# Kernel tuning notes

Measured on AMD Instinct MI355X. Metric: run time of the kernel, lower is better.

## Reference

```python
import jax, jax.numpy as jnp
import numpy as np
from functools import partial

EPS = 1e-5

def batchnorm(x, gamma, beta):
    # training-mode BN over (N,H,W) per channel, NCHW layout
    mean = jnp.mean(x, axis=(0, 2, 3), keepdims=True)
    var = jnp.var(x, axis=(0, 2, 3), keepdims=True)
    xn = (x - mean) * jax.lax.rsqrt(var + EPS)
    return xn * gamma[None, :, None, None] + beta[None, :, None, None]

def ternarize(w):
    # TBN-style per-output-filter ternary quantization: {-a,0,+a}
    absw = jnp.abs(w)
    delta = 0.7 * jnp.mean(absw, axis=(1, 2, 3), keepdims=True)
    mask = (absw > delta).astype(w.dtype)
    alpha = jnp.sum(absw * mask, axis=(1, 2, 3), keepdims=True) / (
        jnp.sum(mask, axis=(1, 2, 3), keepdims=True) + 1e-8)
    return jnp.sign(w) * mask * alpha

def conv(x, w, stride, padding):
    return jax.lax.conv_general_dilated(
        x, w, window_strides=(stride, stride),
        padding=[(padding, padding), (padding, padding)],
        dimension_numbers=("NCHW", "OIHW", "NCHW"))


def setup_inputs() -> dict:
    key = jax.random.key(0)
    ks = jax.random.split(key, 8)
    in_planes, planes, stride = 512, 256, 2
    out_planes = planes * 4
    d = dict(
        x=jax.random.normal(ks[0], (64, in_planes, 28, 28), dtype=jnp.float32),
        bn1_g=jnp.ones((in_planes,), jnp.float32),
        bn1_b=jnp.zeros((in_planes,), jnp.float32),
        w1=jax.random.normal(ks[1], (planes, in_planes, 1, 1), jnp.float32) * 0.05,
        bn2_g=jnp.ones((planes,), jnp.float32),
        bn2_b=jnp.zeros((planes,), jnp.float32),
        w2=jax.random.normal(ks[2], (planes, planes, 3, 3), jnp.float32) * 0.05,
        bn3_g=jnp.ones((planes,), jnp.float32),
        bn3_b=jnp.zeros((planes,), jnp.float32),
        w3=jax.random.normal(ks[3], (out_planes, planes, 1, 1), jnp.float32) * 0.05,
        ds_w=jax.random.normal(ks[4], (out_planes, in_planes, 1, 1), jnp.float32) * 0.05,
        ds_bn_g=jnp.ones((out_planes,), jnp.float32),
        ds_bn_b=jnp.zeros((out_planes,), jnp.float32),
    )
    return d


def reference(x, bn1_g, bn1_b, w1, bn2_g, bn2_b, w2, bn3_g, bn3_b, w3,
              ds_w, ds_bn_g, ds_bn_b):
    stride = 2
    identity = x
    # pre-activation chain: BN -> ternary-quantized conv
    h = conv(batchnorm(x, bn1_g, bn1_b), ternarize(w1), 1, 0)          # [N,256,28,28]
    h = conv(batchnorm(h, bn2_g, bn2_b), ternarize(w2), stride, 1)     # [N,256,14,14]
    h = conv(batchnorm(h, bn3_g, bn3_b), ternarize(w3), 1, 0)          # [N,1024,14,14]
    # downsample(identity, x): projected shortcut + residual add
    sc = batchnorm(conv(identity, ds_w, stride, 0), ds_bn_g, ds_bn_b)
    return h + sc
```

## Files before the change

kernel.cpp:

```cpp
#include <hip/hip_runtime.h>
#include <hip/hip_bf16.h>
#include <math.h>

#define EPS 1e-5f

typedef __hip_bfloat16 bf16;
typedef short short8 __attribute__((ext_vector_type(8)));
typedef float float4v __attribute__((ext_vector_type(4)));

__device__ __forceinline__ float toF(float v) { return v; }
__device__ __forceinline__ float toF(bf16 v) { return __bfloat162float(v); }
__device__ __forceinline__ void stF(float* p, float v) { *p = v; }
__device__ __forceinline__ void stF(bf16* p, float v) { *p = __float2bfloat16(v); }
__device__ __forceinline__ short f2bs(float v) {
    bf16 b = __float2bfloat16(v);
    return *reinterpret_cast<short*>(&b);
}
__device__ __forceinline__ float bs2f(short s) {
    unsigned u = ((unsigned)(unsigned short)s) << 16;
    return __uint_as_float(u);
}

__device__ __forceinline__ float block_reduce_sum(float v) {
    __shared__ float s[256];
    int t = threadIdx.x;
    s[t] = v;
    __syncthreads();
    #pragma unroll
    for (int st = 128; st > 0; st >>= 1) {
        if (t < st) s[t] += s[t + st];
        __syncthreads();
    }
    float r = s[0];
    __syncthreads();
    return r;
}

__global__ void ternarize_kernel(const float* __restrict__ w, short* __restrict__ wt,
                                 float* __restrict__ alpha, int K) {
    int f = blockIdx.x;
    const float* wf = w + (size_t)f * K;
    short* wtf = wt + (size_t)f * K;

    float s = 0.f;
    for (int i = threadIdx.x; i < K; i += blockDim.x) s += fabsf(wf[i]);
    float total = block_reduce_sum(s);
    float delta = 0.7f * total / (float)K;

    float sm = 0.f, cm = 0.f;
    for (int i = threadIdx.x; i < K; i += blockDim.x) {
        float a = fabsf(wf[i]);
        if (a > delta) { sm += a; cm += 1.f; }
    }
    sm = block_reduce_sum(sm);
    cm = block_reduce_sum(cm);
    if (threadIdx.x == 0) alpha[f] = sm / (cm + 1e-8f);

    for (int i = threadIdx.x; i < K; i += blockDim.x) {
        float v = wf[i];
        float a = fabsf(v);
        wtf[i] = (a > delta) ? ((v > 0.f) ? (short)0x3F80 : (short)0xBF80) : (short)0;
    }
}

__global__ void foldbias_kernel(const short* __restrict__ wt, const float* __restrict__ scale,
                                const float* __restrict__ shift, short* __restrict__ wf,
                                float* __restrict__ bias, int K) {
    int f = blockIdx.x;
    float s = 0.f;
    for (int k = threadIdx.x; k < K; k += blockDim.x) {
        float tv = bs2f(wt[(size_t)f * K + k]);
        wf[(size_t)f * K + k] = f2bs(tv * scale[k]);
        s += tv * shift[k];
    }
    s = block_reduce_sum(s);
    if (threadIdx.x == 0) bias[f] = s;
}

__global__ void f2bf_kernel(const float* __restrict__ in, short* __restrict__ out, int n) {
    int i = blockIdx.x * blockDim.x + threadIdx.x;
    if (i < n) out[i] = f2bs(in[i]);
}

template <typename T, int VEC>
__global__ __launch_bounds__(256) void bn_sum_kernel(
    const T* __restrict__ src, float* __restrict__ sum, float* __restrict__ sq,
    int C, int spatial, int N, int splits) {
    int c = blockIdx.x;
    int vpc = spatial / VEC;
    int total = N * vpc;
    float s = 0.f, s2 = 0.f;
    for (int v = blockIdx.y * 256 + threadIdx.x; v < total; v += splits * 256) {
        int n = v / vpc;
        int i = v - n * vpc;
        const T* p = src + ((size_t)n * C + c) * spatial + i * VEC;
        float vals[VEC];
        if (sizeof(T) == 4) {
            float4 q = *(const float4*)p;
            vals[0] = q.x; vals[1] = q.y; vals[2] = q.z; vals[3] = q.w;
        } else {
            short tmp[VEC];
            if (VEC == 8) *(int4*)tmp = *(const int4*)p;
            else          *(int2*)tmp = *(const int2*)p;
            #pragma unroll
            for (int k = 0; k < VEC; k++) vals[k] = bs2f(tmp[k]);
        }
        #pragma unroll
        for (int k = 0; k < VEC; k++) { s += vals[k]; s2 += vals[k] * vals[k]; }
    }
    s = block_reduce_sum(s);
    s2 = block_reduce_sum(s2);
    if (threadIdx.x == 0) {
        atomicAdd(&sum[c], s);
        atomicAdd(&sq[c], s2);
    }
}

__global__ void bn_finalize_kernel(const float* __restrict__ sum, const float* __restrict__ sq,
                                   const float* __restrict__ g, const float* __restrict__ b,
                                   float* __restrict__ scale, float* __restrict__ shift,
                                   int C, float cnt) {
    int c = blockIdx.x * blockDim.x + threadIdx.x;
    if (c >= C) return;
    float mean = sum[c] / cnt;
    float var = fmaxf(sq[c] / cnt - mean * mean, 0.f);
    float r = rsqrtf(var + EPS);
    float sc = g[c] * r;
    scale[c] = sc;
    shift[c] = b[c] - mean * sc;
}

__global__ __launch_bounds__(256) void stats_transpose_kernel(
    const float* __restrict__ in, short* __restrict__ Bt,
    float* __restrict__ sum, float* __restrict__ sq, int C, int SP) {
    __shared__ short tile[64][66];
    __shared__ float rs[4][64], rq[4][64];
    int n = blockIdx.z;
    int ci0 = blockIdx.y * 64;
    int p0 = blockIdx.x * 64;
    int t = threadIdx.x;
    int tx = t & 63;
    int ty4 = t >> 6;

    {
        int p4 = t & 15;
        int cib = t >> 4;
        int p = p0 + p4 * 4;
        bool pok = (p + 3) < SP;
        #pragma unroll
        for (int it = 0; it < 4; it++) {
            int ci = cib + it * 16;
            float4 q;
            if (pok) q = *(const float4*)(in + ((size_t)n * C + ci0 + ci) * SP + p);
            else     q = make_float4(0.f, 0.f, 0.f, 0.f);
            tile[p4 * 4 + 0][ci] = f2bs(q.x);
            tile[p4 * 4 + 1][ci] = f2bs(q.y);
            tile[p4 * 4 + 2][ci] = f2bs(q.z);
            tile[p4 * 4 + 3][ci] = f2bs(q.w);
        }
    }
    __syncthreads();

    {
        int seg = t & 7;
        #pragma unroll
        for (int it = 0; it < 2; it++) {
            int pl = (t >> 3) + it * 32;
            int pw = p0 + pl;
            if (pw < SP) {
                short v[8];
                #pragma unroll
                for (int u = 0; u < 8; u++) v[u] = tile[pl][seg * 8 + u];
                *(int4*)(Bt + ((size_t)n * SP + pw) * C + ci0 + seg * 8) = *(int4*)v;
            }
        }
    }

    float s = 0.f, s2 = 0.f;
    #pragma unroll
    for (int r = 0; r < 16; r++) {
        int pl = ty4 + r * 4;
        int pw = p0 + pl;
        if (pw < SP) {
            float v = bs2f(tile[pl][tx]);
            s += v; s2 += v * v;
        }
    }
    rs[ty4][tx] = s; rq[ty4][tx] = s2;
    __syncthreads();
    if (ty4 == 0) {
        float ts = rs[0][tx] + rs[1][tx] + rs[2][tx] + rs[3][tx];
        float tq = rq[0][tx] + rq[1][tx] + rq[2][tx] + rq[3][tx];
        atomicAdd(&sum[ci0 + tx], ts);
        atomicAdd(&sq[ci0 + tx], tq);
    }
}

__global__ __launch_bounds__(256) void affine_transpose_bf16_kernel(
    const bf16* __restrict__ in, const float* __restrict__ scale,
    const float* __restrict__ shift, short* __restrict__ Bt,
    int C, int SP) {
    __shared__ short tile[64][66];
    int n = blockIdx.z;
    int ci0 = blockIdx.y * 64;
    int p0 = blockIdx.x * 64;
    int t = threadIdx.x;

    {
        int p4 = t & 15;
        int cib = t >> 4;
        int p = p0 + p4 * 4;
        bool pok = (p + 3) < SP;
        #pragma unroll
        for (int it = 0; it < 4; it++) {
            int ci = cib + it * 16;
            short v[4] = {0, 0, 0, 0};
            if (pok) *(int2*)v = *(const int2*)(in + ((size_t)n * C + ci0 + ci) * SP + p);
            float sc = scale[ci0 + ci], sh = shift[ci0 + ci];
            #pragma unroll
            for (int j = 0; j < 4; j++)
                tile[p4 * 4 + j][ci] = f2bs(bs2f(v[j]) * sc + sh);
        }
    }
    __syncthreads();

    {
        int seg = t & 7;
        #pragma unroll
        for (int it = 0; it < 2; it++) {
            int pl = (t >> 3) + it * 32;
            int pw = p0 + pl;
            if (pw < SP) {
                short v[8];
                #pragma unroll
                for (int u = 0; u < 8; u++) v[u] = tile[pl][seg * 8 + u];
                *(int4*)(Bt + ((size_t)n * SP + pw) * C + ci0 + seg * 8) = *(int4*)v;
            }
        }
    }
}

__global__ __launch_bounds__(256) void im2col_tiled_kernel(
    const bf16* __restrict__ h1, const float* __restrict__ scale,
    const float* __restrict__ shift, short* __restrict__ B2t) {
    __shared__ short tile[16][784];
    int cb = blockIdx.x;
    int n  = blockIdx.y;
    int ci0 = cb * 16;
    int t = threadIdx.x;

    for (int v = t; v < 16 * 98; v += 256) {
        int ci = v / 98;
        int i8 = (v - ci * 98) * 8;
        short tmp[8];
        *(int4*)tmp = *(const int4*)(h1 + ((size_t)n * 256 + ci0 + ci) * 784 + i8);
        float sc = scale[ci0 + ci], sh = shift[ci0 + ci];
        short ov[8];
        #pragma unroll
        for (int k = 0; k < 8; k++) ov[k] = f2bs(bs2f(tmp[k]) * sc + sh);
        *(int4*)&tile[ci][i8] = *(int4*)ov;
    }
    __syncthreads();

    for (int w = t; w < 196 * 18; w += 256) {
        int p = w / 18, seg = w - p * 18;
        int oh = p / 14, ow = p - oh * 14;
        int kbase = seg * 8;
        short vals[8];
        #pragma unroll
        for (int u = 0; u < 8; u++) {
            int kk = kbase + u;
            int ci_l = kk / 9;
            int rr = kk - ci_l * 9;
            int kh = rr / 3, kw = rr - kh * 3;
            int ih = 2 * oh - 1 + kh;
            int iw = 2 * ow - 1 + kw;
            vals[u] = ((unsigned)ih < 28u && (unsigned)iw < 28u)
                          ? tile[ci_l][ih * 28 + iw] : (short)0;
        }
        *(int4*)(B2t + ((size_t)(n * 196 + p)) * 2304 + ci0 * 9 + kbase) = *(int4*)vals;
    }
}

template <int SP, typename TOut, bool HAS_ALPHA, bool FUSE, bool HAS_BIAS, bool BREMAP>
__global__ __launch_bounds__(256) void gemm_kernel(
    const short* __restrict__ A, const short* __restrict__ Bt,
    const float* __restrict__ alpha, TOut* __restrict__ out,
    int M, int K,
    const bf16* __restrict__ scv, const float* __restrict__ fscale,
    const float* __restrict__ fshift, const float* __restrict__ bias) {
    __shared__ short As[128 * 32];
    __shared__ short Bs[128 * 32];
    int t = threadIdx.x;
    int c0 = blockIdx.x * 128;
    int m0 = blockIdx.y * 128;
    int w = t >> 6, l = t & 63;
    int wm = (w >> 1) * 64, wn = (w & 1) * 64;

    int r0 = t >> 2;
    int kg = (t & 3) * 8;

    size_t rowB0, rowB1;
    if (BREMAP) {
        int c = c0 + r0;
        int nn = c / 196, pp = c - nn * 196;
        int oh = pp / 14, ow = pp - oh * 14;
        rowB0 = (size_t)nn * 784 + oh * 56 + ow * 2;
        c += 64;
        nn = c / 196; pp = c - nn * 196;
        oh = pp / 14; ow = pp - oh * 14;
        rowB1 = (size_t)nn * 784 + oh * 56 + ow * 2;
    } else {
        rowB0 = c0 + r0;
        rowB1 = c0 + r0 + 64;
    }

    float4v acc[4][4];
    #pragma unroll
    for (int i = 0; i < 4; i++)
        #pragma unroll
        for (int j = 0; j < 4; j++) acc[i][j] = (float4v)0.f;

    int lm = (l >> 4);
    int lc = l & 15;

    for (int k0 = 0; k0 < K; k0 += 32) {
        int4 av0 = *(const int4*)(A + (size_t)(m0 + r0) * K + k0 + kg);
        int4 av1 = *(const int4*)(A + (size_t)(m0 + r0 + 64) * K + k0 + kg);
        int4 bv0 = *(const int4*)(Bt + rowB0 * K + k0 + kg);
        int4 bv1 = *(const int4*)(Bt + rowB1 * K + k0 + kg);
        __syncthreads();
        *(int4*)&As[r0 * 32 + kg] = av0;
        *(int4*)&As[(r0 + 64) * 32 + kg] = av1;
        *(int4*)&Bs[r0 * 32 + kg] = bv0;
        *(int4*)&Bs[(r0 + 64) * 32 + kg] = bv1;
        __syncthreads();

        short8 af[4], bfr[4];
        #pragma unroll
        for (int i = 0; i < 4; i++)
            af[i] = *(const short8*)&As[(wm + i * 16 + lc) * 32 + lm * 8];
        #pragma unroll
        for (int j = 0; j < 4; j++)
            bfr[j] = *(const short8*)&Bs[(wn + j * 16 + lc) * 32 + lm * 8];
        #pragma unroll
        for (int i = 0; i < 4; i++)
            #pragma unroll
            for (int j = 0; j < 4; j++)
                acc[i][j] = __builtin_amdgcn_mfma_f32_16x16x32_bf16(af[i], bfr[j], acc[i][j], 0, 0, 0);
    }

    #pragma unroll
    for (int i = 0; i < 4; i++) {
        #pragma unroll
        for (int r = 0; r < 4; r++) {
            int m = m0 + wm + i * 16 + lm * 4 + r;
            float a = HAS_ALPHA ? alpha[m] : 1.f;
            float bia = HAS_BIAS ? bias[m] : 0.f;
            float fsc = FUSE ? fscale[m] : 0.f;
            float fsh = FUSE ? fshift[m] : 0.f;
            #pragma unroll
            for (int j = 0; j < 4; j++) {
                int c = c0 + wn + j * 16 + lc;
                int n = c / SP;
                int p = c - n * SP;
                size_t idx = ((size_t)n * M + m) * SP + p;
                float v = acc[i][j][r];
                if (HAS_BIAS) v += bia;
                if (HAS_ALPHA) v *= a;
                if (FUSE) v += toF(scv[idx]) * fsc + fsh;
                stF(&out[idx], v);
            }
        }
    }
}

extern "C" void kernel_launch(void* const* d_in, const int* in_sizes, int n_in,
                              void* d_out, int out_size, void* d_ws, size_t ws_size,
                              hipStream_t stream) {
    const float* x      = (const float*)d_in[0];
    const float* bn1_g  = (const float*)d_in[1];
    const float* bn1_b  = (const float*)d_in[2];
    const float* w1     = (const float*)d_in[3];
    const float* bn2_g  = (const float*)d_in[4];
    const float* bn2_b  = (const float*)d_in[5];
    const float* w2     = (const float*)d_in[6];
    const float* bn3_g  = (const float*)d_in[7];
    const float* bn3_b  = (const float*)d_in[8];
    const float* w3     = (const float*)d_in[9];
    const float* ds_w   = (const float*)d_in[10];
    const float* dbn_g  = (const float*)d_in[11];
    const float* dbn_b  = (const float*)d_in[12];
    float* out = (float*)d_out;

    const int N = 64, C1 = 512, C2 = 256, C3 = 1024;
    const int SP1 = 784, SP2 = 196;
    const int NT1 = N * SP1;
    const int NT2 = N * SP2;

    char* wsb = (char*)d_ws;
    size_t off = 0;
    auto alloc = [&](size_t bytes) { char* p = wsb + off; off += (bytes + 255) & ~(size_t)255; return p; };

    char* pool = alloc((size_t)NT2 * 2304 * 2);
    short* B1t = (short*)pool;
    short* B2t = (short*)pool;
    short* B3t = (short*)pool;
    bf16*  sc  = (bf16*)alloc((size_t)N * C3 * SP2 * 2);

    bf16* h1 = (bf16*)alloc((size_t)N * C2 * SP1 * 2);
    bf16* h2 = (bf16*)alloc((size_t)N * C2 * SP2 * 2);
    short* w1t  = (short*)alloc((size_t)C2 * C1 * 2);
    short* w1f  = (short*)alloc((size_t)C2 * C1 * 2);
    short* w2t  = (short*)alloc((size_t)C2 * C2 * 9 * 2);
    short* w3t  = (short*)alloc((size_t)C3 * C2 * 2);
    short* dswb = (short*)alloc((size_t)C3 * C1 * 2);
    float* alpha1 = (float*)alloc(C2 * 4);
    float* alpha2 = (float*)alloc(C2 * 4);
    float* alpha3 = (float*)alloc(C3 * 4);
    float* bias1  = (float*)alloc(C2 * 4);
    float* scale1 = (float*)alloc(C1 * 4);
    float* shift1 = (float*)alloc(C1 * 4);
    float* scale2 = (float*)alloc(C2 * 4);
    float* shift2 = (float*)alloc(C2 * 4);
    float* scale3 = (float*)alloc(C2 * 4);
    float* shift3 = (float*)alloc(C2 * 4);
    float* scaled = (float*)alloc(C3 * 4);
    float* shiftd = (float*)alloc(C3 * 4);
    float* acc_base = (float*)alloc((size_t)(C1 + C2 + C2 + C3) * 2 * 4);
    float* sum1 = acc_base;            float* sq1 = sum1 + C1;
    float* sum2 = sq1 + C1;            float* sq2 = sum2 + C2;
    float* sum3 = sq2 + C2;            float* sq3 = sum3 + C2;
    float* sumd = sq3 + C2;            float* sqd = sumd + C3;
    (void)ws_size; (void)in_sizes; (void)n_in; (void)out_size;

    hipMemsetAsync(acc_base, 0, (size_t)(C1 + C2 + C2 + C3) * 2 * 4, stream);

    ternarize_kernel<<<C2, 256, 0, stream>>>(w1, w1t, alpha1, C1);
    ternarize_kernel<<<C2, 256, 0, stream>>>(w2, w2t, alpha2, C2 * 9);
    ternarize_kernel<<<C3, 256, 0, stream>>>(w3, w3t, alpha3, C2);
    f2bf_kernel<<<(C3 * C1 + 255) / 256, 256, 0, stream>>>(ds_w, dswb, C3 * C1);

    {
        dim3 grid((SP1 + 63) / 64, C1 / 64, N);
        stats_transpose_kernel<<<grid, 256, 0, stream>>>(x, B1t, sum1, sq1, C1, SP1);
    }
    bn_finalize_kernel<<<(C1 + 255) / 256, 256, 0, stream>>>(sum1, sq1, bn1_g, bn1_b,
                                                             scale1, shift1, C1, (float)(N * SP1));
    foldbias_kernel<<<C2, 256, 0, stream>>>(w1t, scale1, shift1, w1f, bias1, C1);

    gemm_kernel<784, bf16, true, false, true, false><<<dim3(NT1 / 128, C2 / 128), 256, 0, stream>>>(
        w1f, B1t, alpha1, h1, C2, C1, nullptr, nullptr, nullptr, bias1);

    gemm_kernel<196, bf16, false, false, false, true><<<dim3(NT2 / 128, C3 / 128), 256, 0, stream>>>(
        dswb, B1t, nullptr, sc, C3, C1, nullptr, nullptr, nullptr, nullptr);

    bn_sum_kernel<bf16, 4><<<dim3(C3, 4), 256, 0, stream>>>(sc, sumd, sqd, C3, SP2, N, 4);
    bn_finalize_kernel<<<(C3 + 255) / 256, 256, 0, stream>>>(sumd, sqd, dbn_g, dbn_b,
                                                             scaled, shiftd, C3, (float)(N * SP2));

    bn_sum_kernel<bf16, 8><<<dim3(C2, 8), 256, 0, stream>>>(h1, sum2, sq2, C2, SP1, N, 8);
    bn_finalize_kernel<<<(C2 + 255) / 256, 256, 0, stream>>>(sum2, sq2, bn2_g, bn2_b,
                                                             scale2, shift2, C2, (float)(N * SP1));
    im2col_tiled_kernel<<<dim3(16, 64), 256, 0, stream>>>(h1, scale2, shift2, B2t);

    gemm_kernel<196, bf16, true, false, false, false><<<dim3(NT2 / 128, C2 / 128), 256, 0, stream>>>(
        w2t, B2t, alpha2, h2, C2, C2 * 9, nullptr, nullptr, nullptr, nullptr);

    bn_sum_kernel<bf16, 4><<<dim3(C2, 4), 256, 0, stream>>>(h2, sum3, sq3, C2, SP2, N, 4);
    bn_finalize_kernel<<<(C2 + 255) / 256, 256, 0, stream>>>(sum3, sq3, bn3_g, bn3_b,
                                                             scale3, shift3, C2, (float)(N * SP2));
    {
        dim3 grid((SP2 + 63) / 64, C2 / 64, N);
        affine_transpose_bf16_kernel<<<grid, 256, 0, stream>>>(
            h2, scale3, shift3, B3t, C2, SP2);
    }

    gemm_kernel<196, float, true, true, false, false><<<dim3(NT2 / 128, C3 / 128), 256, 0, stream>>>(
        w3t, B3t, alpha3, out, C3, C2, sc, scaled, shiftd, nullptr);
}
```

Before: 441.8 us.

## Prefetch next K-tile into registers, pad LDS rows, use smaller tiles for conv2 GEMM

```diff
diff --git a/kernel.cpp b/kernel.cpp
--- a/kernel.cpp
+++ b/kernel.cpp
@@ -282,76 +282,93 @@
     }
 }
 
-template <int SP, typename TOut, bool HAS_ALPHA, bool FUSE, bool HAS_BIAS, bool BREMAP>
+template <int BM, int BN, int SP, typename TOut, bool HAS_ALPHA, bool FUSE, bool HAS_BIAS, bool BREMAP>
 __global__ __launch_bounds__(256) void gemm_kernel(
     const short* __restrict__ A, const short* __restrict__ Bt,
     const float* __restrict__ alpha, TOut* __restrict__ out,
     int M, int K,
     const bf16* __restrict__ scv, const float* __restrict__ fscale,
     const float* __restrict__ fshift, const float* __restrict__ bias) {
-    __shared__ short As[128 * 32];
-    __shared__ short Bs[128 * 32];
+    constexpr int BKP = 40;
+    constexpr int WM = BM / 2, WN = BN / 2;
+    constexpr int MI = WM / 16, NJ = WN / 16;
+    constexpr int RA = BM / 64, RB = BN / 64;
+    __shared__ short As[BM * BKP];
+    __shared__ short Bs[BN * BKP];
     int t = threadIdx.x;
-    int c0 = blockIdx.x * 128;
-    int m0 = blockIdx.y * 128;
+    int c0 = blockIdx.x * BN;
+    int m0 = blockIdx.y * BM;
     int w = t >> 6, l = t & 63;
-    int wm = (w >> 1) * 64, wn = (w & 1) * 64;
+    int wm = (w >> 1) * WM, wn = (w & 1) * WN;
 
     int r0 = t >> 2;
     int kg = (t & 3) * 8;
 
-    size_t rowB0, rowB1;
-    if (BREMAP) {
-        int c = c0 + r0;
-        int nn = c / 196, pp = c - nn * 196;
-        int oh = pp / 14, ow = pp - oh * 14;
-        rowB0 = (size_t)nn * 784 + oh * 56 + ow * 2;
-        c += 64;
-        nn = c / 196; pp = c - nn * 196;
-        oh = pp / 14; ow = pp - oh * 14;
-        rowB1 = (size_t)nn * 784 + oh * 56 + ow * 2;
-    } else {
-        rowB0 = c0 + r0;
-        rowB1 = c0 + r0 + 64;
-    }
-
-    float4v acc[4][4];
-    #pragma unroll
-    for (int i = 0; i < 4; i++)
-        #pragma unroll
-        for (int j = 0; j < 4; j++) acc[i][j] = (float4v)0.f;
+    size_t rowB[RB];
+    #pragma unroll
+    for (int rr = 0; rr < RB; rr++) {
+        int c = c0 + r0 + rr * 64;
+        if (BREMAP) {
+            int nn = c / 196, pp = c - nn * 196;
+            int oh = pp / 14, ow = pp - oh * 14;
+            rowB[rr] = (size_t)nn * 784 + oh * 56 + ow * 2;
+        } else {
+            rowB[rr] = c;
+        }
+    }
+
+    float4v acc[MI][NJ];
+    #pragma unroll
+    for (int i = 0; i < MI; i++)
+        #pragma unroll
+        for (int j = 0; j < NJ; j++) acc[i][j] = (float4v)0.f;
 
     int lm = (l >> 4);
     int lc = l & 15;
 
+    int4 av[RA], bv[RB];
+    #pragma unroll
+    for (int rr = 0; rr < RA; rr++)
+        av[rr] = *(const int4*)(A + (size_t)(m0 + r0 + rr * 64) * K + kg);
+    #pragma unroll
+    for (int rr = 0; rr < RB; rr++)
+        bv[rr] = *(const int4*)(Bt + rowB[rr] * K + kg);
+
     for (int k0 = 0; k0 < K; k0 += 32) {
-        int4 av0 = *(const int4*)(A + (size_t)(m0 + r0) * K + k0 + kg);
-        int4 av1 = *(const int4*)(A + (size_t)(m0 + r0 + 64) * K + k0 + kg);
-        int4 bv0 = *(const int4*)(Bt + rowB0 * K + k0 + kg);
-        int4 bv1 = *(const int4*)(Bt + rowB1 * K + k0 + kg);
         __syncthreads();
-        *(int4*)&As[r0 * 32 + kg] = av0;
-        *(int4*)&As[(r0 + 64) * 32 + kg] = av1;
-        *(int4*)&Bs[r0 * 32 + kg] = bv0;
-        *(int4*)&Bs[(r0 + 64) * 32 + kg] = bv1;
+        #pragma unroll
+        for (int rr = 0; rr < RA; rr++)
+            *(int4*)&As[(r0 + rr * 64) * BKP + kg] = av[rr];
+        #pragma unroll
+        for (int rr = 0; rr < RB; rr++)
+            *(int4*)&Bs[(r0 + rr * 64) * BKP + kg] = bv[rr];
         __syncthreads();
 
-        short8 af[4], bfr[4];
-        #pragma unroll
-        for (int i = 0; i < 4; i++)
-            af[i] = *(const short8*)&As[(wm + i * 16 + lc) * 32 + lm * 8];
-        #pragma unroll
-        for (int j = 0; j < 4; j++)
-            bfr[j] = *(const short8*)&Bs[(wn + j * 16 + lc) * 32 + lm * 8];
-        #pragma unroll
-        for (int i = 0; i < 4; i++)
+        if (k0 + 32 < K) {
             #pragma unroll
-            for (int j = 0; j < 4; j++)
+            for (int rr = 0; rr < RA; rr++)
+                av[rr] = *(const int4*)(A + (size_t)(m0 + r0 + rr * 64) * K + k0 + 32 + kg);
+            #pragma unroll
+            for (int rr = 0; rr < RB; rr++)
+                bv[rr] = *(const int4*)(Bt + rowB[rr] * K + k0 + 32 + kg);
+        }
+
+        short8 af[MI], bfr[NJ];
+        #pragma unroll
+        for (int i = 0; i < MI; i++)
+            af[i] = *(const short8*)&As[(wm + i * 16 + lc) * BKP + lm * 8];
+        #pragma unroll
+        for (int j = 0; j < NJ; j++)
+            bfr[j] = *(const short8*)&Bs[(wn + j * 16 + lc) * BKP + lm * 8];
+        #pragma unroll
+        for (int i = 0; i < MI; i++)
+            #pragma unroll
+            for (int j = 0; j < NJ; j++)
                 acc[i][j] = __builtin_amdgcn_mfma_f32_16x16x32_bf16(af[i], bfr[j], acc[i][j], 0, 0, 0);
     }
 
     #pragma unroll
-    for (int i = 0; i < 4; i++) {
+    for (int i = 0; i < MI; i++) {
         #pragma unroll
         for (int r = 0; r < 4; r++) {
             int m = m0 + wm + i * 16 + lm * 4 + r;
@@ -360,7 +377,7 @@
             float fsc = FUSE ? fscale[m] : 0.f;
             float fsh = FUSE ? fshift[m] : 0.f;
             #pragma unroll
-            for (int j = 0; j < 4; j++) {
+            for (int j = 0; j < NJ; j++) {
                 int c = c0 + wn + j * 16 + lc;
                 int n = c / SP;
                 int p = c - n * SP;
@@ -449,10 +466,12 @@
                                                              scale1, shift1, C1, (float)(N * SP1));
     foldbias_kernel<<<C2, 256, 0, stream>>>(w1t, scale1, shift1, w1f, bias1, C1);
 
-    gemm_kernel<784, bf16, true, false, true, false><<<dim3(NT1 / 128, C2 / 128), 256, 0, stream>>>(
+    gemm_kernel<128, 128, 784, bf16, true, false, true, false>
+        <<<dim3(NT1 / 128, C2 / 128), 256, 0, stream>>>(
         w1f, B1t, alpha1, h1, C2, C1, nullptr, nullptr, nullptr, bias1);
 
-    gemm_kernel<196, bf16, false, false, false, true><<<dim3(NT2 / 128, C3 / 128), 256, 0, stream>>>(
+    gemm_kernel<128, 128, 196, bf16, false, false, false, true>
+        <<<dim3(NT2 / 128, C3 / 128), 256, 0, stream>>>(
         dswb, B1t, nullptr, sc, C3, C1, nullptr, nullptr, nullptr, nullptr);
 
     bn_sum_kernel<bf16, 4><<<dim3(C3, 4), 256, 0, stream>>>(sc, sumd, sqd, C3, SP2, N, 4);
@@ -464,7 +483,8 @@
                                                              scale2, shift2, C2, (float)(N * SP1));
     im2col_tiled_kernel<<<dim3(16, 64), 256, 0, stream>>>(h1, scale2, shift2, B2t);
 
-    gemm_kernel<196, bf16, true, false, false, false><<<dim3(NT2 / 128, C2 / 128), 256, 0, stream>>>(
+    gemm_kernel<64, 64, 196, bf16, true, false, false, false>
+        <<<dim3(NT2 / 64, C2 / 64), 256, 0, stream>>>(
         w2t, B2t, alpha2, h2, C2, C2 * 9, nullptr, nullptr, nullptr, nullptr);
 
     bn_sum_kernel<bf16, 4><<<dim3(C2, 4), 256, 0, stream>>>(h2, sum3, sq3, C2, SP2, N, 4);
@@ -476,6 +496,7 @@
             h2, scale3, shift3, B3t, C2, SP2);
     }
 
-    gemm_kernel<196, float, true, true, false, false><<<dim3(NT2 / 128, C3 / 128), 256, 0, stream>>>(
+    gemm_kernel<128, 128, 196, float, true, true, false, false>
+        <<<dim3(NT2 / 128, C3 / 128), 256, 0, stream>>>(
         w3t, B3t, alpha3, out, C3, C2, sc, scaled, shiftd, nullptr);
 }
```

Result: slower. 542.5 us (+22.8%).
